# Kernel optimization log

Measured on AMD Instinct MI355X. Metric: run time of the kernel, lower is better.

The kernel has to match this reference:

```python
import jax, jax.numpy as jnp
from jax import lax
import numpy as np

WSTD = 0.1
BSTD = 0.1
DN = ("NHWC", "HWIO", "NHWC")  # matches tf.nn.convolution defaults


def setup_inputs() -> dict:
    key = jax.random.key(0)
    k1, k2, k3, k4, k5 = jax.random.split(key, 5)
    B, H, Wd, Cin, F, KH, KW = 32, 64, 64, 128, 256, 3, 3
    X = jax.random.normal(k1, (B, H, Wd, Cin), dtype=jnp.float32)
    # glorot-ish kernel
    fan = KH * KW * Cin
    W = jax.random.normal(k2, (KH, KW, Cin, F), dtype=jnp.float32) / np.float32(np.sqrt(fan))
    bias = 0.01 * jax.random.normal(k3, (F,), dtype=jnp.float32)
    # per-sample multiplicative errors: abs(1 + N(0, std)) as in A-Connect
    Werr = jnp.abs(1.0 + WSTD * jax.random.normal(k4, (B, KH, KW, Cin, F), dtype=jnp.float32))
    Berr = jnp.abs(1.0 + BSTD * jax.random.normal(k5, (B, F), dtype=jnp.float32))
    return {"X": X, "W": W, "bias": bias, "Werr": Werr, "Berr": Berr}


def reference(X, W, bias, Werr, Berr):
    # memW[b] = W * Werr[b]  -> per-sample perturbed kernels [B,KH,KW,Cin,F]
    memW = W[None] * Werr

    def conv1(x, k):  # x: [H,W,Cin], k: [KH,KW,Cin,F]
        return lax.conv_general_dilated(x[None], k, window_strides=(1, 1),
                                        padding="SAME", dimension_numbers=DN)[0]

    Z = jax.vmap(conv1)(X, memW)                 # [B,H,W,F]
    membias = bias[None] * Berr                  # [B,F]
    Z = Z + membias[:, None, None, :]
    return jax.nn.relu(Z)
```

## Files before the change

### kernel.cpp

```cpp
#include <hip/hip_runtime.h>

#define B_   32
#define H_   64
#define W_   64
#define CIN  128
#define F_   256
#define K_   1152
#define M_   4096

#define HP_   66
#define XPROW (66*128)
#define XPIMG (66*66*128)
#define XP_ELEMS ((size_t)B_ * XPIMG)
#define XP_BYTES (XP_ELEMS * 2)

#define WBT_BYTES ((size_t)B_ * F_ * K_ * 2)
#define FULL_WS   (WBT_BYTES + XP_BYTES + 256)
#define ZPAGE_OFF WBT_BYTES

typedef __attribute__((ext_vector_type(8))) short bf16x8;
typedef __attribute__((ext_vector_type(4))) float f32x4;

__device__ __forceinline__ unsigned pkbf(float a, float b) {
    unsigned ua = __builtin_bit_cast(unsigned, a) + 0x8000u;
    unsigned ub = __builtin_bit_cast(unsigned, b) + 0x8000u;
    return __builtin_amdgcn_perm(ub, ua, 0x07060302u);
}

__device__ __forceinline__ void async16(const void* g, void* l) {
    __builtin_amdgcn_global_load_lds(
        (const __attribute__((address_space(1))) unsigned int*)g,
        (__attribute__((address_space(3))) unsigned int*)l, 16, 0, 0);
}

__global__ void wbt_kernel(const float* __restrict__ W,
                           const float* __restrict__ Werr,
                           unsigned short* __restrict__ WbT,
                           unsigned int* __restrict__ zpage) {
    __shared__ float tile[32 * 68];
    int bid = blockIdx.x;
    int ft   = bid & 3;
    int rest = bid >> 2;
    int kt   = rest % 36;
    int b    = rest / 36;
    int k0 = kt * 32;
    int f0 = ft * 64;
    int t  = threadIdx.x;

    if (bid == 0 && t < 64) zpage[t] = 0u;

    #pragma unroll
    for (int i = 0; i < 2; ++i) {
        int c   = i * 256 + t;
        int kl  = c >> 4;
        int fl4 = c & 15;
        size_t src = (size_t)(k0 + kl) * F_ + f0 + fl4 * 4;
        f32x4 w4 = *(const f32x4*)&W[src];
        f32x4 e4 = *(const f32x4*)&Werr[(size_t)b * (K_ * F_) + src];
        f32x4 v  = w4 * e4;
        *(f32x4*)&tile[kl * 68 + fl4 * 4] = v;
    }
    __syncthreads();
    {
        int c  = t;
        int fl = c >> 2;
        int ku = c & 3;
        unsigned pk[4];
        #pragma unroll
        for (int j2 = 0; j2 < 4; ++j2) {
            float x0 = tile[(ku * 8 + j2 * 2 + 0) * 68 + fl];
            float x1 = tile[(ku * 8 + j2 * 2 + 1) * 68 + fl];
            pk[j2] = pkbf(x0, x1);
        }
        size_t dst = ((size_t)(b * F_ + f0 + fl)) * K_ + k0 + ku * 8;
        *(uint4*)&WbT[dst] = make_uint4(pk[0], pk[1], pk[2], pk[3]);
    }
}

__global__ void xp_kernel(const float* __restrict__ X,
                          unsigned short* __restrict__ Xp) {
    int e = blockIdx.x * 256 + threadIdx.x;
    int c16  = e & 15;
    int pos  = e >> 4;
    int wp   = pos % 66;
    int rest = pos / 66;
    int hp   = rest % 66;
    int b    = rest / 66;
    uint4 out;
    if (hp >= 1 && hp <= 64 && wp >= 1 && wp <= 64) {
        const float* src = X + (((size_t)b * 64 + (hp - 1)) * 64 + (wp - 1)) * 128
                             + c16 * 8;
        f32x4 a = *(const f32x4*)src;
        f32x4 c = *(const f32x4*)(src + 4);
        out.x = pkbf(a[0], a[1]);  out.y = pkbf(a[2], a[3]);
        out.z = pkbf(c[0], c[1]);  out.w = pkbf(c[2], c[3]);
    } else {
        out = make_uint4(0u, 0u, 0u, 0u);
    }
    *(uint4*)&Xp[(size_t)e * 8] = out;
}

__global__ __launch_bounds__(256, 2)
void gemm_kernel(const unsigned short* __restrict__ Xp,
                 const unsigned short* __restrict__ WbT,
                 const float* __restrict__ bias,
                 const float* __restrict__ Berr,
                 float* __restrict__ Out) {
    __shared__ unsigned short As[128 * 32];
    __shared__ unsigned short Bs[128 * 32];

    int bid = blockIdx.x;
    int g   = (bid & 7) | ((bid >> 8) << 3);
    int mt  = (bid >> 3) & 31;
    int b   = g >> 1;
    int nt  = g & 1;
    int pm0 = mt * 128;

    int t    = threadIdx.x;
    int lane = t & 63;
    int wv   = t >> 6;
    int wm   = wv >> 1;
    int wn   = wv & 1;
    int l16  = lane & 15;
    int quad = lane >> 4;

    const unsigned short* Abase[2];
    #pragma unroll
    for (int cc = 0; cc < 2; ++cc) {
        int c   = t + cc * 256;
        int ml  = c >> 2;
        int off = c & 3;
        int m   = pm0 + ml;
        int hb  = m >> 6;
        int ww  = m & 63;
        Abase[cc] = Xp + (size_t)b * XPIMG + (size_t)hb * XPROW
                       + (size_t)ww * 128 + off * 8;
    }

    const unsigned short* wb = WbT + ((size_t)(b * F_ + nt * 128)) * K_;
    const unsigned short* Bbase[2];
    #pragma unroll
    for (int cc = 0; cc < 2; ++cc) {
        int c   = t + cc * 256;
        int nl  = c >> 2;
        int off = c & 3;
        Bbase[cc] = wb + (size_t)nl * K_ + off * 8;
    }

    f32x4 acc[4][4];
    #pragma unroll
    for (int mi = 0; mi < 4; ++mi)
        #pragma unroll
        for (int ni = 0; ni < 4; ++ni)
            acc[mi][ni] = (f32x4){0.f, 0.f, 0.f, 0.f};

    for (int kt = 0; kt < 36; ++kt) {
        int khw   = kt >> 2;
        int kh    = (khw * 11) >> 5;
        int kw    = khw - kh * 3;
        int koffA = kh * XPROW + kw * 128 + ((kt & 3) << 5);
        int koffB = kt * 32;

        if (kt) __syncthreads();
        async16(Abase[0] + koffA, &As[t * 8]);
        async16(Abase[1] + koffA, &As[(t + 256) * 8]);
        async16(Bbase[0] + koffB, &Bs[t * 8]);
        async16(Bbase[1] + koffB, &Bs[(t + 256) * 8]);
        __syncthreads();

        bf16x8 af[4], bf[4];
        #pragma unroll
        for (int i = 0; i < 4; ++i) {
            af[i] = *(const bf16x8*)&As[(wm * 64 + i * 16 + l16) * 32 + quad * 8];
            bf[i] = *(const bf16x8*)&Bs[(wn * 64 + i * 16 + l16) * 32 + quad * 8];
        }
        #pragma unroll
        for (int mi = 0; mi < 4; ++mi)
            #pragma unroll
            for (int ni = 0; ni < 4; ++ni)
                acc[mi][ni] = __builtin_amdgcn_mfma_f32_16x16x32_bf16(
                    af[mi], bf[ni], acc[mi][ni], 0, 0, 0);
    }

    float mb[4];
    #pragma unroll
    for (int ni = 0; ni < 4; ++ni) {
        int f = nt * 128 + wn * 64 + ni * 16 + l16;
        mb[ni] = bias[f] * Berr[b * F_ + f];
    }
    #pragma unroll
    for (int mi = 0; mi < 4; ++mi) {
        #pragma unroll
        for (int rr = 0; rr < 4; ++rr) {
            int mm = pm0 + wm * 64 + mi * 16 + quad * 4 + rr;
            float* orow = Out + ((size_t)b * M_ + mm) * F_ + nt * 128 + wn * 64;
            #pragma unroll
            for (int ni = 0; ni < 4; ++ni) {
                float v = acc[mi][ni][rr] + mb[ni];
                orow[ni * 16 + l16] = fmaxf(v, 0.0f);
            }
        }
    }
}

__global__ __launch_bounds__(256, 2)
void gemm_kernel_f32(const float* __restrict__ X,
                     const unsigned short* __restrict__ WbT,
                     const float* __restrict__ zpage,
                     const float* __restrict__ bias,
                     const float* __restrict__ Berr,
                     float* __restrict__ Out) {
    __shared__ unsigned short As[128 * 32];
    __shared__ unsigned short Bs[128 * 32];

    int bid = blockIdx.x;
    int g   = (bid & 7) | ((bid >> 8) << 3);
    int mt  = (bid >> 3) & 31;
    int b   = g >> 1;
    int nt  = g & 1;
    int pm0 = mt * 128;

    int t    = threadIdx.x;
    int lane = t & 63;
    int wv   = t >> 6;
    int wm   = wv >> 1;
    int wn   = wv & 1;
    int l16  = lane & 15;
    int quad = lane >> 4;

    int ml   = t >> 1;
    int half = t & 1;
    int m    = pm0 + ml;
    int hb   = m >> 6;
    int wwv  = m & 63;
    const float* Abase = X + (((size_t)b * 64 + hb - 1) * 64 + (wwv - 1)) * 128
                           + half * 16;
    unsigned vm = 0;
    #pragma unroll
    for (int khw = 0; khw < 9; ++khw) {
        int kh = (khw * 11) >> 5;
        int kw = khw - kh * 3;
        bool ok = ((unsigned)(hb + kh - 1) < 64u) && ((unsigned)(wwv + kw - 1) < 64u);
        vm |= (unsigned)ok << khw;
    }
    int ldsA = ml * 32 + half * 16;

    const unsigned short* wb = WbT + ((size_t)(b * F_ + nt * 128)) * K_;
    const unsigned short* Bbase[2];
    int ldsB[2];
    #pragma unroll
    for (int cc = 0; cc < 2; ++cc) {
        int c   = t + cc * 256;
        int nl  = c >> 2;
        int off = c & 3;
        Bbase[cc] = wb + (size_t)nl * K_ + off * 8;
        ldsB[cc]  = c * 8;
    }

    f32x4 acc[4][4];
    #pragma unroll
    for (int mi = 0; mi < 4; ++mi)
        #pragma unroll
        for (int ni = 0; ni < 4; ++ni)
            acc[mi][ni] = (f32x4){0.f, 0.f, 0.f, 0.f};

    f32x4 pr0, pr1, pr2, pr3;
    {
        const float* p = (vm & 1) ? Abase : zpage;
        pr0 = *(const f32x4*)(p);
        pr1 = *(const f32x4*)(p + 4);
        pr2 = *(const f32x4*)(p + 8);
        pr3 = *(const f32x4*)(p + 12);
    }

    for (int kt = 0; kt < 36; ++kt) {
        uint4 lo, hi;
        lo.x = pkbf(pr0[0], pr0[1]);  lo.y = pkbf(pr0[2], pr0[3]);
        lo.z = pkbf(pr1[0], pr1[1]);  lo.w = pkbf(pr1[2], pr1[3]);
        hi.x = pkbf(pr2[0], pr2[1]);  hi.y = pkbf(pr2[2], pr2[3]);
        hi.z = pkbf(pr3[0], pr3[1]);  hi.w = pkbf(pr3[2], pr3[3]);

        if (kt) __syncthreads();
        *(uint4*)&As[ldsA]     = lo;
        *(uint4*)&As[ldsA + 8] = hi;
        #pragma unroll
        for (int cc = 0; cc < 2; ++cc)
            async16(Bbase[cc] + kt * 32, &Bs[ldsB[cc]]);
        __syncthreads();

        if (kt < 35) {
            int ktn  = kt + 1;
            int khw  = ktn >> 2;
            int kh   = (khw * 11) >> 5;
            int kw   = khw - kh * 3;
            int koff = kh * 8192 + kw * 128 + ((ktn & 3) << 5);
            const float* p = ((vm >> khw) & 1) ? Abase + koff : zpage;
            pr0 = *(const f32x4*)(p);
            pr1 = *(const f32x4*)(p + 4);
            pr2 = *(const f32x4*)(p + 8);
            pr3 = *(const f32x4*)(p + 12);
        }

        bf16x8 af[4], bf[4];
        #pragma unroll
        for (int i = 0; i < 4; ++i) {
            af[i] = *(const bf16x8*)&As[(wm * 64 + i * 16 + l16) * 32 + quad * 8];
            bf[i] = *(const bf16x8*)&Bs[(wn * 64 + i * 16 + l16) * 32 + quad * 8];
        }
        #pragma unroll
        for (int mi = 0; mi < 4; ++mi)
            #pragma unroll
            for (int ni = 0; ni < 4; ++ni)
                acc[mi][ni] = __builtin_amdgcn_mfma_f32_16x16x32_bf16(
                    af[mi], bf[ni], acc[mi][ni], 0, 0, 0);
    }

    float mb[4];
    #pragma unroll
    for (int ni = 0; ni < 4; ++ni) {
        int f = nt * 128 + wn * 64 + ni * 16 + l16;
        mb[ni] = bias[f] * Berr[b * F_ + f];
    }
    #pragma unroll
    for (int mi = 0; mi < 4; ++mi) {
        #pragma unroll
        for (int rr = 0; rr < 4; ++rr) {
            int mm = pm0 + wm * 64 + mi * 16 + quad * 4 + rr;
            float* orow = Out + ((size_t)b * M_ + mm) * F_ + nt * 128 + wn * 64;
            #pragma unroll
            for (int ni = 0; ni < 4; ++ni) {
                float v = acc[mi][ni][rr] + mb[ni];
                orow[ni * 16 + l16] = fmaxf(v, 0.0f);
            }
        }
    }
}

__global__ __launch_bounds__(256)
void fallback_kernel(const float* __restrict__ X, const float* __restrict__ W,
                     const float* __restrict__ bias, const float* __restrict__ Werr,
                     const float* __restrict__ Berr, float* __restrict__ Out) {
    __shared__ float Xs[3 * 66 * 128];
    int bid = blockIdx.x;
    int b = bid >> 6;
    int h = bid & 63;
    int t = threadIdx.x;
    int f = t;

    for (int e = t; e < 3 * 66 * 128; e += 256) {
        int kh  = e / (66 * 128);
        int rem = e - kh * 66 * 128;
        int w66 = rem >> 7;
        int c   = rem & 127;
        int hh = h + kh - 1, ww = w66 - 1;
        float v = 0.f;
        if (hh >= 0 && hh < 64 && ww >= 0 && ww < 64)
            v = X[(((size_t)b * 64 + hh) * 64 + ww) * 128 + c];
        Xs[e] = v;
    }
    __syncthreads();

    float acc[64];
    #pragma unroll
    for (int w = 0; w < 64; ++w) acc[w] = 0.f;

    for (int kk = 0; kk < 9; ++kk) {
        int kh = (kk * 11) >> 5;
        int kw = kk - kh * 3;
        for (int c = 0; c < 128; ++c) {
            size_t wi = ((size_t)kk * 128 + c) * 256 + f;
            float wvv = W[wi] * Werr[(size_t)b * (K_ * F_) + wi];
            const float* xr = &Xs[(kh * 66 + kw) * 128 + c];
            #pragma unroll
            for (int w = 0; w < 64; ++w)
                acc[w] = fmaf(xr[w * 128], wvv, acc[w]);
        }
    }
    float mb = bias[f] * Berr[b * 256 + f];
    for (int w = 0; w < 64; ++w)
        Out[(((size_t)b * 64 + h) * 64 + w) * 256 + f] = fmaxf(acc[w] + mb, 0.f);
}

extern "C" void kernel_launch(void* const* d_in, const int* in_sizes, int n_in,
                              void* d_out, int out_size, void* d_ws, size_t ws_size,
                              hipStream_t stream) {
    const float* X    = (const float*)d_in[0];
    const float* W    = (const float*)d_in[1];
    const float* bias = (const float*)d_in[2];
    const float* Werr = (const float*)d_in[3];
    const float* Berr = (const float*)d_in[4];
    float* Out = (float*)d_out;

    if (ws_size >= FULL_WS) {
        unsigned short* WbT = (unsigned short*)d_ws;
        unsigned short* Xp  = (unsigned short*)((char*)d_ws + WBT_BYTES);
        unsigned int*   zpg = (unsigned int*)((char*)d_ws + WBT_BYTES + XP_BYTES);
        wbt_kernel<<<B_ * 36 * 4, 256, 0, stream>>>(W, Werr, WbT, zpg);
        xp_kernel<<<8712, 256, 0, stream>>>(X, Xp);
        gemm_kernel<<<B_ * 32 * 2, 256, 0, stream>>>(Xp, WbT, bias, Berr, Out);
    } else if (ws_size >= WBT_BYTES + 256) {
        unsigned short* WbT  = (unsigned short*)d_ws;
        unsigned int*   zpg  = (unsigned int*)((char*)d_ws + ZPAGE_OFF);
        wbt_kernel<<<B_ * 36 * 4, 256, 0, stream>>>(W, Werr, WbT, zpg);
        gemm_kernel_f32<<<B_ * 32 * 2, 256, 0, stream>>>(X, WbT, (const float*)zpg,
                                                         bias, Berr, Out);
    } else {
        fallback_kernel<<<B_ * 64, 256, 0, stream>>>(X, W, bias, Werr, Berr, Out);
    }
}
```

Measured before the change: 313.3 us.

## Fuse prep kernels and use 256x256 double-buffered swizzled GEMM tiles

Merges the weight-perturb/transposition and input-padding kernels into one launch. Replaces the 128x128x32 GEMM with a 256x256x64 tile on 512 threads: full F per block, XOR-swizzled LDS and double-buffered async global-to-LDS loads that prefetch the next K slice during MFMA work. It also raises MFMA priority with s_setprio and remaps blocks so the same sample's tiles run together. The aim is fewer launches, more operand reuse per byte loaded and hidden load latency, at the cost of larger LDS use, higher register pressure and only 512 blocks.

```diff
diff --git a/kernel.cpp b/kernel.cpp
--- a/kernel.cpp
+++ b/kernel.cpp
@@ -18,6 +18,9 @@
 #define FULL_WS   (WBT_BYTES + XP_BYTES + 256)
 #define ZPAGE_OFF WBT_BYTES
 
+#define BM_ 256
+#define BK_ 64
+
 typedef __attribute__((ext_vector_type(8))) short bf16x8;
 typedef __attribute__((ext_vector_type(4))) float f32x4;
 
@@ -31,6 +34,75 @@
     __builtin_amdgcn_global_load_lds(
         (const __attribute__((address_space(1))) unsigned int*)g,
         (__attribute__((address_space(3))) unsigned int*)l, 16, 0, 0);
+}
+
+__global__ void prep_kernel(const float* __restrict__ W,
+                            const float* __restrict__ Werr,
+                            const float* __restrict__ X,
+                            unsigned short* __restrict__ WbT,
+                            unsigned short* __restrict__ Xp,
+                            unsigned int* __restrict__ zpage) {
+    __shared__ float tile[32 * 68];
+    int bid = blockIdx.x;
+    int t   = threadIdx.x;
+
+    if (bid < 4608) {
+        int ft   = bid & 3;
+        int rest = bid >> 2;
+        int kt   = rest % 36;
+        int b    = rest / 36;
+        int k0 = kt * 32;
+        int f0 = ft * 64;
+
+        if (bid == 0 && t < 64) zpage[t] = 0u;
+
+        #pragma unroll
+        for (int i = 0; i < 2; ++i) {
+            int c   = i * 256 + t;
+            int kl  = c >> 4;
+            int fl4 = c & 15;
+            size_t src = (size_t)(k0 + kl) * F_ + f0 + fl4 * 4;
+            f32x4 w4 = *(const f32x4*)&W[src];
+            f32x4 e4 = *(const f32x4*)&Werr[(size_t)b * (K_ * F_) + src];
+            f32x4 v  = w4 * e4;
+            *(f32x4*)&tile[kl * 68 + fl4 * 4] = v;
+        }
+        __syncthreads();
+        {
+            int c  = t;
+            int fl = c >> 2;
+            int ku = c & 3;
+            unsigned pk[4];
+            #pragma unroll
+            for (int j2 = 0; j2 < 4; ++j2) {
+                float x0 = tile[(ku * 8 + j2 * 2 + 0) * 68 + fl];
+                float x1 = tile[(ku * 8 + j2 * 2 + 1) * 68 + fl];
+                pk[j2] = pkbf(x0, x1);
+            }
+            size_t dst = ((size_t)(b * F_ + f0 + fl)) * K_ + k0 + ku * 8;
+            *(uint4*)&WbT[dst] = make_uint4(pk[0], pk[1], pk[2], pk[3]);
+        }
+    } else {
+        int e = (bid - 4608) * 256 + t;
+        int c16  = e & 15;
+        int pos  = e >> 4;
+        int wp   = pos % 66;
+        int rest = pos / 66;
+        int hp   = rest % 66;
+        int b    = rest / 66;
+        uint4 out;
+        if (hp >= 1 && hp <= 64 && wp >= 1 && wp <= 64) {
+            const float* src = X + (((size_t)b * 64 + (hp - 1)) * 64 + (wp - 1)) * 128
+                                 + c16 * 8;
+            f32x4 a = *(const f32x4*)src;
+            f32x4 c = *(const f32x4*)(src + 4);
+            out.x = pkbf(a[0], a[1]);  out.y = pkbf(a[2], a[3]);
+            out.z = pkbf(c[0], c[1]);  out.w = pkbf(c[2], c[3]);
+        } else {
+            out = make_uint4(0u, 0u, 0u, 0u);
+        }
+        *(uint4*)&Xp[(size_t)e * 8] = out;
+    }
 }
 
 __global__ void wbt_kernel(const float* __restrict__ W,
@@ -77,123 +149,144 @@
     }
 }
 
-__global__ void xp_kernel(const float* __restrict__ X,
-                          unsigned short* __restrict__ Xp) {
-    int e = blockIdx.x * 256 + threadIdx.x;
-    int c16  = e & 15;
-    int pos  = e >> 4;
-    int wp   = pos % 66;
-    int rest = pos / 66;
-    int hp   = rest % 66;
-    int b    = rest / 66;
-    uint4 out;
-    if (hp >= 1 && hp <= 64 && wp >= 1 && wp <= 64) {
-        const float* src = X + (((size_t)b * 64 + (hp - 1)) * 64 + (wp - 1)) * 128
-                             + c16 * 8;
-        f32x4 a = *(const f32x4*)src;
-        f32x4 c = *(const f32x4*)(src + 4);
-        out.x = pkbf(a[0], a[1]);  out.y = pkbf(a[2], a[3]);
-        out.z = pkbf(c[0], c[1]);  out.w = pkbf(c[2], c[3]);
-    } else {
-        out = make_uint4(0u, 0u, 0u, 0u);
-    }
-    *(uint4*)&Xp[(size_t)e * 8] = out;
-}
-
-__global__ __launch_bounds__(256, 2)
-void gemm_kernel(const unsigned short* __restrict__ Xp,
-                 const unsigned short* __restrict__ WbT,
-                 const float* __restrict__ bias,
-                 const float* __restrict__ Berr,
-                 float* __restrict__ Out) {
-    __shared__ unsigned short As[128 * 32];
-    __shared__ unsigned short Bs[128 * 32];
+__global__ __launch_bounds__(512, 2)
+void gemm256_kernel(const unsigned short* __restrict__ Xp,
+                    const unsigned short* __restrict__ WbT,
+                    const float* __restrict__ bias,
+                    const float* __restrict__ Berr,
+                    float* __restrict__ Out) {
+    __shared__ unsigned short As[2][BM_ * BK_];
+    __shared__ unsigned short Bs[2][BM_ * BK_];
 
     int bid = blockIdx.x;
-    int g   = (bid & 7) | ((bid >> 8) << 3);
-    int mt  = (bid >> 3) & 31;
-    int b   = g >> 1;
-    int nt  = g & 1;
-    int pm0 = mt * 128;
+    int g   = (bid & 7) * 64 + (bid >> 3);
+    int b   = g >> 4;
+    int mt  = g & 15;
+    int pm0 = mt * 256;
 
     int t    = threadIdx.x;
     int lane = t & 63;
     int wv   = t >> 6;
-    int wm   = wv >> 1;
-    int wn   = wv & 1;
+    int wm   = wv >> 2;
+    int wn   = wv & 3;
     int l16  = lane & 15;
     int quad = lane >> 4;
-
-    const unsigned short* Abase[2];
-    #pragma unroll
-    for (int cc = 0; cc < 2; ++cc) {
-        int c   = t + cc * 256;
-        int ml  = c >> 2;
-        int off = c & 3;
-        int m   = pm0 + ml;
-        int hb  = m >> 6;
-        int ww  = m & 63;
-        Abase[cc] = Xp + (size_t)b * XPIMG + (size_t)hb * XPROW
-                       + (size_t)ww * 128 + off * 8;
-    }
-
-    const unsigned short* wb = WbT + ((size_t)(b * F_ + nt * 128)) * K_;
-    const unsigned short* Bbase[2];
-    #pragma unroll
-    for (int cc = 0; cc < 2; ++cc) {
-        int c   = t + cc * 256;
-        int nl  = c >> 2;
-        int off = c & 3;
-        Bbase[cc] = wb + (size_t)nl * K_ + off * 8;
-    }
-
-    f32x4 acc[4][4];
-    #pragma unroll
-    for (int mi = 0; mi < 4; ++mi)
+    int swz  = (l16 & 7) << 4;
+
+    const unsigned short* XpB = Xp + (size_t)b * XPIMG;
+    const unsigned short* WbB = WbT + (size_t)b * F_ * K_;
+
+    int aofs[4], bofs[4], ldst[4];
+    #pragma unroll
+    for (int p = 0; p < 4; ++p) {
+        int c   = p * 512 + t;
+        int row = c >> 3;
+        int col = c & 7;
+        int sc  = col ^ (row & 7);
+        int m   = pm0 + row;
+        int hb  = m >> 6, ww = m & 63;
+        aofs[p] = hb * XPROW + ww * 128 + sc * 8;
+        bofs[p] = row * K_ + sc * 8;
+        ldst[p] = c * 8;
+    }
+
+    f32x4 acc[8][4];
+    #pragma unroll
+    for (int mi = 0; mi < 8; ++mi)
         #pragma unroll
         for (int ni = 0; ni < 4; ++ni)
             acc[mi][ni] = (f32x4){0.f, 0.f, 0.f, 0.f};
 
-    for (int kt = 0; kt < 36; ++kt) {
-        int khw   = kt >> 2;
-        int kh    = (khw * 11) >> 5;
-        int kw    = khw - kh * 3;
-        int koffA = kh * XPROW + kw * 128 + ((kt & 3) << 5);
-        int koffB = kt * 32;
-
-        if (kt) __syncthreads();
-        async16(Abase[0] + koffA, &As[t * 8]);
-        async16(Abase[1] + koffA, &As[(t + 256) * 8]);
-        async16(Bbase[0] + koffB, &Bs[t * 8]);
-        async16(Bbase[1] + koffB, &Bs[(t + 256) * 8]);
-        __syncthreads();
-
-        bf16x8 af[4], bf[4];
-        #pragma unroll
-        for (int i = 0; i < 4; ++i) {
-            af[i] = *(const bf16x8*)&As[(wm * 64 + i * 16 + l16) * 32 + quad * 8];
-            bf[i] = *(const bf16x8*)&Bs[(wn * 64 + i * 16 + l16) * 32 + quad * 8];
-        }
-        #pragma unroll
-        for (int mi = 0; mi < 4; ++mi)
+    #pragma unroll
+    for (int p = 0; p < 4; ++p)
+        async16(XpB + aofs[p], &As[0][ldst[p]]);
+    #pragma unroll
+    for (int p = 0; p < 4; ++p)
+        async16(WbB + bofs[p], &Bs[0][ldst[p]]);
+    asm volatile("s_waitcnt vmcnt(0)" ::: "memory");
+    __builtin_amdgcn_s_barrier();
+
+    for (int kt = 0; kt < 18; ++kt) {
+        const int cur = kt & 1;
+        const unsigned short* Acur = As[cur];
+        const unsigned short* Bcur = Bs[cur];
+        unsigned short* Anxt = As[cur ^ 1];
+        unsigned short* Bnxt = Bs[cur ^ 1];
+        const bool pf = (kt < 17);
+
+        int ktn  = kt + 1;
+        int khwN = ktn >> 1;
+        int khN  = (khwN * 11) >> 5;
+        int kwN  = khwN - khN * 3;
+        int koA  = khN * XPROW + kwN * 128 + (ktn & 1) * 64;
+        int koB  = ktn * 64;
+
+        bf16x8 bfr[4];
+        #pragma unroll
+        for (int ks = 0; ks < 2; ++ks) {
             #pragma unroll
-            for (int ni = 0; ni < 4; ++ni)
-                acc[mi][ni] = __builtin_amdgcn_mfma_f32_16x16x32_bf16(
-                    af[mi], bf[ni], acc[mi][ni], 0, 0, 0);
+            for (int qm = 0; qm < 2; ++qm) {
+                if (qm == 0) {
+                    #pragma unroll
+                    for (int ni = 0; ni < 4; ++ni) {
+                        int row = wn * 64 + ni * 16 + l16;
+                        bfr[ni] = *(const bf16x8*)((const char*)Bcur +
+                                   ((row * 128 + quad * 16 + ks * 64) ^ swz));
+                    }
+                }
+                bf16x8 af[4];
+                #pragma unroll
+                for (int mi = 0; mi < 4; ++mi) {
+                    int row = wm * 128 + (qm * 4 + mi) * 16 + l16;
+                    af[mi] = *(const bf16x8*)((const char*)Acur +
+                              ((row * 128 + quad * 16 + ks * 64) ^ swz));
+                }
+
+                if (pf && ks == 0) {
+                    if (qm == 0) {
+                        #pragma unroll
+                        for (int p = 0; p < 4; ++p)
+                            async16(XpB + aofs[p] + koA, &Anxt[ldst[p]]);
+                    } else {
+                        #pragma unroll
+                        for (int p = 0; p < 4; ++p)
+                            async16(WbB + bofs[p] + koB, &Bnxt[ldst[p]]);
+                    }
+                }
+
+                __builtin_amdgcn_s_barrier();
+
+                __builtin_amdgcn_s_setprio(1);
+                #pragma unroll
+                for (int mi = 0; mi < 4; ++mi)
+                    #pragma unroll
+                    for (int ni = 0; ni < 4; ++ni)
+                        acc[qm * 4 + mi][ni] = __builtin_amdgcn_mfma_f32_16x16x32_bf16(
+                            af[mi], bfr[ni], acc[qm * 4 + mi][ni], 0, 0, 0);
+                __builtin_amdgcn_s_setprio(0);
+
+                if (ks == 1 && qm == 1) {
+                    if (pf) asm volatile("s_waitcnt vmcnt(0)" ::: "memory");
+                    __builtin_amdgcn_s_barrier();
+                } else {
+                    __builtin_amdgcn_s_barrier();
+                }
+            }
+        }
     }
 
     float mb[4];
     #pragma unroll
     for (int ni = 0; ni < 4; ++ni) {
-        int f = nt * 128 + wn * 64 + ni * 16 + l16;
+        int f = wn * 64 + ni * 16 + l16;
         mb[ni] = bias[f] * Berr[b * F_ + f];
     }
     #pragma unroll
-    for (int mi = 0; mi < 4; ++mi) {
+    for (int mi = 0; mi < 8; ++mi) {
         #pragma unroll
         for (int rr = 0; rr < 4; ++rr) {
-            int mm = pm0 + wm * 64 + mi * 16 + quad * 4 + rr;
-            float* orow = Out + ((size_t)b * M_ + mm) * F_ + nt * 128 + wn * 64;
+            int mm = pm0 + wm * 128 + mi * 16 + quad * 4 + rr;
+            float* orow = Out + ((size_t)b * M_ + mm) * F_ + wn * 64;
             #pragma unroll
             for (int ni = 0; ni < 4; ++ni) {
                 float v = acc[mi][ni][rr] + mb[ni];
@@ -395,9 +488,8 @@
         unsigned short* WbT = (unsigned short*)d_ws;
         unsigned short* Xp  = (unsigned short*)((char*)d_ws + WBT_BYTES);
         unsigned int*   zpg = (unsigned int*)((char*)d_ws + WBT_BYTES + XP_BYTES);
-        wbt_kernel<<<B_ * 36 * 4, 256, 0, stream>>>(W, Werr, WbT, zpg);
-        xp_kernel<<<8712, 256, 0, stream>>>(X, Xp);
-        gemm_kernel<<<B_ * 32 * 2, 256, 0, stream>>>(Xp, WbT, bias, Berr, Out);
+        prep_kernel<<<4608 + 8712, 256, 0, stream>>>(W, Werr, X, WbT, Xp, zpg);
+        gemm256_kernel<<<512, 512, 0, stream>>>(Xp, WbT, bias, Berr, Out);
     } else if (ws_size >= WBT_BYTES + 256) {
         unsigned short* WbT  = (unsigned short*)d_ws;
         unsigned int*   zpg  = (unsigned int*)((char*)d_ws + ZPAGE_OFF);
```

Result: no change. 311.2 us (-0.7%).
